# Kernel tuning notes

Measured on AMD Instinct MI355X. Metric: run time of the kernel, lower is better.

The kernel has to match this reference:

```python
import jax, jax.numpy as jnp
import numpy as np

NUM_ITERS = 15
EPSILON = 0.05
MESH_ITERS = 3


def _cost_proj(x, W1, b1, W2, b2):
    # Linear -> ReLU -> Linear
    h = jax.nn.relu(x @ W1 + b1)
    return h @ W2 + b2


def setup_inputs() -> dict:
    key = jax.random.key(0)
    ks = jax.random.split(key, 4)
    B, K, M, D = 8192, 32, 32, 256
    s = 1.0 / np.sqrt(D)
    return {
        "slots_q": jax.random.normal(ks[0], (B, K, D), dtype=jnp.float32),
        "slots_r": jax.random.normal(ks[1], (B, M, D), dtype=jnp.float32),
        "W1": (jax.random.normal(ks[2], (D, D), dtype=jnp.float32) * s),
        "b1": jnp.zeros((D,), dtype=jnp.float32),
        "W2": (jax.random.normal(ks[3], (D, D), dtype=jnp.float32) * s),
        "b2": jnp.zeros((D,), dtype=jnp.float32),
    }


def reference(slots_q, slots_r, W1, b1, W2, b2):
    q = _cost_proj(slots_q, W1, b1, W2, b2)  # [B,K,D]
    r = _cost_proj(slots_r, W1, b1, W2, b2)  # [B,M,D]
    # torch.cdist p=2: pairwise euclidean distance
    sq = (jnp.sum(q * q, -1)[:, :, None]
          + jnp.sum(r * r, -1)[:, None, :]
          - 2.0 * jnp.einsum('bkd,bmd->bkm', q, r))
    C = jnp.sqrt(jnp.clip(sq, 0.0))  # [B,K,M]
    B, K, M = C.shape
    log_K = -C / EPSILON
    log_a = jnp.zeros((B, K, 1), dtype=C.dtype)
    log_b = jnp.zeros((B, 1, M), dtype=C.dtype)
    for _ in range(NUM_ITERS):
        log_a = -jax.nn.logsumexp(log_K + log_b, axis=2, keepdims=True)
        log_b = -jax.nn.logsumexp(log_K + log_a, axis=1, keepdims=True)
    T = jnp.exp(log_K + log_a + log_b)
    for _ in range(MESH_ITERS):
        T = T ** 2
        T = T / (jnp.sum(T, axis=-1, keepdims=True) + 1e-8)
        T = T / (jnp.sum(T, axis=-2, keepdims=True) + 1e-8)
    cost = jnp.sum(T * C, axis=(-1, -2))  # [B]
    similarity = jax.nn.sigmoid(-cost)
    return similarity, T, C, cost
```

## Files before the change

kernel.cpp:

```cpp
#include <hip/hip_runtime.h>


typedef unsigned short u16;
typedef short short8 __attribute__((ext_vector_type(8)));
typedef float f32x4  __attribute__((ext_vector_type(4)));

#define MFMA(a, b, c) __builtin_amdgcn_mfma_f32_16x16x32_bf16((a), (b), (c), 0, 0, 0)

static __device__ __forceinline__ u16 f2bf(float f) {
  unsigned u = __float_as_uint(f);
  return (u16)((u + 0x7FFFu + ((u >> 16) & 1u)) >> 16);
}
static __device__ __forceinline__ float bf2f(u16 h) {
  return __uint_as_float(((unsigned)h) << 16);
}

__global__ __launch_bounds__(256) void prep_w(const float* __restrict__ W1,
                                              const float* __restrict__ W2,
                                              u16* __restrict__ ws) {
  int id = blockIdx.x * 256 + threadIdx.x;
  int mat = id >> 16;
  int e = id & 65535;
  int k = e >> 8, n = e & 255;
  float wv = (mat ? W2 : W1)[e];
  int ki = k >> 5, kl = k & 31;
  int g = kl >> 3, j = kl & 7;
  int lane = g * 16 + (n & 15);
  int ctg = n >> 4;
  ws[mat * 65536 + ((((ki * 16 + ctg) * 64 + lane) << 3) | j)] = f2bf(wv);
}

struct __align__(16) SMemA {
  u16 F[16384];
  float nrm[64];
};

static __device__ __forceinline__ void gemm_frag(const u16* __restrict__ Af,
                                                 const u16* __restrict__ wf,
                                                 int w, int lane, f32x4 acc[4][2]) {
#pragma unroll
  for (int rt = 0; rt < 4; ++rt) {
    acc[rt][0] = f32x4{0.f, 0.f, 0.f, 0.f};
    acc[rt][1] = f32x4{0.f, 0.f, 0.f, 0.f};
  }
#pragma unroll
  for (int ki = 0; ki < 8; ++ki) {
    const u16* bp = wf + (((ki * 16 + 2 * w) * 64 + lane) << 3);
    short8 b0 = *reinterpret_cast<const short8*>(bp);
    short8 b1 = *reinterpret_cast<const short8*>(bp + 512);
    short8 a[4];
#pragma unroll
    for (int rt = 0; rt < 4; ++rt)
      a[rt] = *reinterpret_cast<const short8*>(Af + (((ki * 4 + rt) * 64 + lane) << 3));
#pragma unroll
    for (int rt = 0; rt < 4; ++rt) {
      acc[rt][0] = MFMA(a[rt], b0, acc[rt][0]);
      acc[rt][1] = MFMA(a[rt], b1, acc[rt][1]);
    }
  }
}

__global__ __launch_bounds__(512, 8) void gemm_cdist(
    const float* __restrict__ slots_q, const float* __restrict__ slots_r,
    const float* __restrict__ b1, const float* __restrict__ b2,
    const u16* __restrict__ ws, float* __restrict__ CO) {
  __shared__ SMemA sm;
  const int tid = threadIdx.x, b = blockIdx.x;
  const int w = tid >> 6, lane = tid & 63, g = lane >> 4, ln = lane & 15;

  {
    const float* srcq = slots_q + (size_t)b * 8192;
    const float* srcr = slots_r + (size_t)b * 8192;
#pragma unroll
    for (int ii = 0; ii < 4; ++ii) {
      int s = tid + ii * 512;
      int ki = s >> 8, rt = (s >> 6) & 3, sg = (s >> 4) & 3, sln = s & 15;
      int row = rt * 16 + sln;
      const float* src = (row < 32) ? (srcq + row * 256) : (srcr + (row - 32) * 256);
      int k0 = ki * 32 + sg * 8;
      float4 v0 = *reinterpret_cast<const float4*>(src + k0);
      float4 v1 = *reinterpret_cast<const float4*>(src + k0 + 4);
      short8 o;
      o[0] = (short)f2bf(v0.x); o[1] = (short)f2bf(v0.y);
      o[2] = (short)f2bf(v0.z); o[3] = (short)f2bf(v0.w);
      o[4] = (short)f2bf(v1.x); o[5] = (short)f2bf(v1.y);
      o[6] = (short)f2bf(v1.z); o[7] = (short)f2bf(v1.w);
      *reinterpret_cast<short8*>(&sm.F[s << 3]) = o;
    }
  }
  float bv1a = b1[32 * w + ln], bv1b = b1[32 * w + 16 + ln];
  float bv2a = b2[32 * w + ln], bv2b = b2[32 * w + 16 + ln];
  __syncthreads();

  f32x4 acc[4][2];
  gemm_frag(sm.F, ws, w, lane, acc);
  __syncthreads();
#pragma unroll
  for (int ct = 0; ct < 2; ++ct) {
    float bv = ct ? bv1b : bv1a;
#pragma unroll
    for (int rt = 0; rt < 4; ++rt)
#pragma unroll
      for (int ri = 0; ri < 4; ++ri) {
        int lane2 = (2 * ct + (ln >> 3)) * 16 + 4 * g + ri;
        sm.F[(((w * 4 + rt) * 64 + lane2) << 3) | (ln & 7)] =
            f2bf(fmaxf(acc[rt][ct][ri] + bv, 0.0f));
      }
  }
  __syncthreads();

  gemm_frag(sm.F, ws + 65536, w, lane, acc);
  __syncthreads();
#pragma unroll
  for (int ct = 0; ct < 2; ++ct) {
    float bv = ct ? bv2b : bv2a;
#pragma unroll
    for (int rt = 0; rt < 4; ++rt)
#pragma unroll
      for (int ri = 0; ri < 4; ++ri) {
        int lane2 = (2 * ct + (ln >> 3)) * 16 + 4 * g + ri;
        sm.F[(((w * 4 + rt) * 64 + lane2) << 3) | (ln & 7)] =
            f2bf(acc[rt][ct][ri] + bv);
      }
  }
  __syncthreads();

  f32x4 dacc = f32x4{0.f, 0.f, 0.f, 0.f};
  if (w < 4) {
    const int mt = w >> 1, nt = w & 1;
#pragma unroll
    for (int ki = 0; ki < 8; ++ki) {
      short8 aq = *reinterpret_cast<const short8*>(
          &sm.F[(((ki * 4 + mt) * 64 + lane) << 3)]);
      short8 br = *reinterpret_cast<const short8*>(
          &sm.F[(((ki * 4 + 2 + nt) * 64 + lane) << 3)]);
      dacc = MFMA(aq, br, dacc);
    }
  } else {
    const int t = w - 4;
    float s = 0.f;
#pragma unroll
    for (int ki = 0; ki < 8; ++ki) {
      short8 v = *reinterpret_cast<const short8*>(
          &sm.F[(((ki * 4 + t) * 64 + lane) << 3)]);
#pragma unroll
      for (int i = 0; i < 8; ++i) {
        float f = bf2f((u16)v[i]);
        s = fmaf(f, f, s);
      }
    }
    s += __shfl_xor(s, 16);
    s += __shfl_xor(s, 32);
    if (lane < 16) sm.nrm[t * 16 + lane] = s;
  }
  __syncthreads();

  if (w < 4) {
    const int mt = w >> 1, nt = w & 1;
    float* Cp = CO + (size_t)b * 1024;
#pragma unroll
    for (int ri = 0; ri < 4; ++ri) {
      int k = mt * 16 + 4 * g + ri;
      int m = nt * 16 + ln;
      float sq = sm.nrm[k] + sm.nrm[32 + m] - 2.0f * dacc[ri];
      Cp[k * 32 + m] = sqrtf(fmaxf(sq, 0.0f));
    }
  }
}

__global__ __launch_bounds__(256, 4) void sinkhorn_mesh(
    const float* __restrict__ CO, float* __restrict__ simO,
    float* __restrict__ TO, float* __restrict__ costO, int Bn) {
  __shared__ float Wl[4][32 * 33];
  __shared__ float ABl[4][64];
  const int wv = threadIdx.x >> 6, lane = threadIdx.x & 63;
  const int p = blockIdx.x * 4 + wv;
  if (p >= Bn) return;
  const int h = lane >> 5, q = lane & 31;
  float* Wm = Wl[wv];
  float* LA = ABl[wv];
  float* LB = ABl[wv] + 32;
  const float* Cp = CO + (size_t)p * 1024;

  float lkr[16], lkc[16];
#pragma unroll
  for (int jj = 0; jj < 4; ++jj) {
    float4 v = *reinterpret_cast<const float4*>(Cp + q * 32 + h * 16 + jj * 4);
    int base = q * 33 + h * 16 + jj * 4;
    Wm[base + 0] = v.x; Wm[base + 1] = v.y; Wm[base + 2] = v.z; Wm[base + 3] = v.w;
    lkr[jj * 4 + 0] = -20.f * v.x; lkr[jj * 4 + 1] = -20.f * v.y;
    lkr[jj * 4 + 2] = -20.f * v.z; lkr[jj * 4 + 3] = -20.f * v.w;
  }
  LB[q] = 0.0f;
  __builtin_amdgcn_wave_barrier();
#pragma unroll
  for (int j = 0; j < 16; ++j) lkc[j] = -20.f * Wm[(h * 16 + j) * 33 + q];

  for (int it = 0; it < 15; ++it) {
    float v[16], mx, s;
#pragma unroll
    for (int j = 0; j < 16; ++j) v[j] = lkr[j] + LB[h * 16 + j];
    mx = v[0];
#pragma unroll
    for (int j = 1; j < 16; ++j) mx = fmaxf(mx, v[j]);
    mx = fmaxf(mx, __shfl_xor(mx, 32));
    s = 0.f;
#pragma unroll
    for (int j = 0; j < 16; ++j) s += __expf(v[j] - mx);
    s += __shfl_xor(s, 32);
    LA[q] = -(mx + __logf(s));
    __builtin_amdgcn_wave_barrier();
#pragma unroll
    for (int j = 0; j < 16; ++j) v[j] = lkc[j] + LA[h * 16 + j];
    mx = v[0];
#pragma unroll
    for (int j = 1; j < 16; ++j) mx = fmaxf(mx, v[j]);
    mx = fmaxf(mx, __shfl_xor(mx, 32));
    s = 0.f;
#pragma unroll
    for (int j = 0; j < 16; ++j) s += __expf(v[j] - mx);
    s += __shfl_xor(s, 32);
    LB[q] = -(mx + __logf(s));
    __builtin_amdgcn_wave_barrier();
  }

  float t[16];
  {
    float la = LA[q];
#pragma unroll
    for (int j = 0; j < 16; ++j) t[j] = __expf(lkr[j] + la + LB[h * 16 + j]);
  }

  for (int mi = 0; mi < 3; ++mi) {
    float s = 0.f;
#pragma unroll
    for (int j = 0; j < 16; ++j) { t[j] *= t[j]; s += t[j]; }
    s += __shfl_xor(s, 32);
    float inv = 1.0f / (s + 1e-8f);
#pragma unroll
    for (int j = 0; j < 16; ++j) Wm[q * 33 + h * 16 + j] = t[j] * inv;
    __builtin_amdgcn_wave_barrier();
#pragma unroll
    for (int j = 0; j < 16; ++j) t[j] = Wm[(h * 16 + j) * 33 + q];
    s = 0.f;
#pragma unroll
    for (int j = 0; j < 16; ++j) s += t[j];
    s += __shfl_xor(s, 32);
    inv = 1.0f / (s + 1e-8f);
#pragma unroll
    for (int j = 0; j < 16; ++j) Wm[(h * 16 + j) * 33 + q] = t[j] * inv;
    __builtin_amdgcn_wave_barrier();
#pragma unroll
    for (int j = 0; j < 16; ++j) t[j] = Wm[q * 33 + h * 16 + j];
  }

  float pp = 0.f;
#pragma unroll
  for (int j = 0; j < 16; ++j) pp = fmaf(t[j], -0.05f * lkr[j], pp);
  pp += __shfl_xor(pp, 1); pp += __shfl_xor(pp, 2); pp += __shfl_xor(pp, 4);
  pp += __shfl_xor(pp, 8); pp += __shfl_xor(pp, 16); pp += __shfl_xor(pp, 32);
  if (lane == 0) {
    costO[p] = pp;
    simO[p] = 1.0f / (1.0f + __expf(pp));
  }
#pragma unroll
  for (int jj = 0; jj < 4; ++jj) {
    float4 o;
    o.x = t[jj * 4 + 0]; o.y = t[jj * 4 + 1];
    o.z = t[jj * 4 + 2]; o.w = t[jj * 4 + 3];
    *reinterpret_cast<float4*>(TO + (size_t)p * 1024 + q * 32 + h * 16 + jj * 4) = o;
  }
}

extern "C" void kernel_launch(void* const* d_in, const int* in_sizes, int n_in,
                              void* d_out, int out_size, void* d_ws, size_t ws_size,
                              hipStream_t stream) {
  const float* slots_q = (const float*)d_in[0];
  const float* slots_r = (const float*)d_in[1];
  const float* W1 = (const float*)d_in[2];
  const float* b1 = (const float*)d_in[3];
  const float* W2 = (const float*)d_in[4];
  const float* b2 = (const float*)d_in[5];
  float* out = (float*)d_out;

  const int Bn = in_sizes[0] / 8192;
  u16* ws = (u16*)d_ws;

  prep_w<<<dim3(512), dim3(256), 0, stream>>>(W1, W2, ws);

  float* simO = out;
  float* TO = out + Bn;
  float* CO = TO + (size_t)Bn * 1024;
  float* costO = CO + (size_t)Bn * 1024;

  gemm_cdist<<<dim3(Bn), dim3(512), 0, stream>>>(slots_q, slots_r, b1, b2, ws, CO);
  sinkhorn_mesh<<<dim3((Bn + 3) / 4), dim3(256), 0, stream>>>(CO, simO, TO, costO, Bn);
}
```

Before: 261.6 us.

## Process four batches per block with register-prefetched input and MFMA priority

Result: slower. 815.8 us (+211.8%).

```diff
diff --git a/kernel.cpp b/kernel.cpp
--- a/kernel.cpp
+++ b/kernel.cpp
@@ -43,6 +43,7 @@
     acc[rt][0] = f32x4{0.f, 0.f, 0.f, 0.f};
     acc[rt][1] = f32x4{0.f, 0.f, 0.f, 0.f};
   }
+  __builtin_amdgcn_s_setprio(1);
 #pragma unroll
   for (int ki = 0; ki < 8; ++ki) {
     const u16* bp = wf + (((ki * 16 + 2 * w) * 64 + lane) << 3);
@@ -58,112 +59,138 @@
       acc[rt][1] = MFMA(a[rt], b1, acc[rt][1]);
     }
   }
-}
-
-__global__ __launch_bounds__(512, 8) void gemm_cdist(
+  __builtin_amdgcn_s_setprio(0);
+}
+
+__global__ __launch_bounds__(512, 6) void gemm_cdist(
     const float* __restrict__ slots_q, const float* __restrict__ slots_r,
     const float* __restrict__ b1, const float* __restrict__ b2,
-    const u16* __restrict__ ws, float* __restrict__ CO) {
+    const u16* __restrict__ ws, float* __restrict__ CO, int Bn) {
   __shared__ SMemA sm;
-  const int tid = threadIdx.x, b = blockIdx.x;
+  const int tid = threadIdx.x;
   const int w = tid >> 6, lane = tid & 63, g = lane >> 4, ln = lane & 15;
 
-  {
-    const float* srcq = slots_q + (size_t)b * 8192;
-    const float* srcr = slots_r + (size_t)b * 8192;
+  const int pb0 = blockIdx.x * 4;
+  if (pb0 >= Bn) return;
+  const int npb = (Bn - pb0 < 4) ? (Bn - pb0) : 4;
+
+  const float bv1a = b1[32 * w + ln], bv1b = b1[32 * w + 16 + ln];
+  const float bv2a = b2[32 * w + ln], bv2b = b2[32 * w + 16 + ln];
+
+  const float* sp[4];
+#pragma unroll
+  for (int ii = 0; ii < 4; ++ii) {
+    int s = tid + ii * 512;
+    int ki = s >> 8, rt = (s >> 6) & 3, sg = (s >> 4) & 3, sln = s & 15;
+    int row = rt * 16 + sln;
+    int k0 = ki * 32 + sg * 8;
+    sp[ii] = ((row < 32) ? (slots_q + row * 256) : (slots_r + (row - 32) * 256)) +
+             (size_t)pb0 * 8192 + k0;
+  }
+
+  float4 fl[8];
+#pragma unroll
+  for (int ii = 0; ii < 4; ++ii) {
+    fl[2 * ii]     = *reinterpret_cast<const float4*>(sp[ii]);
+    fl[2 * ii + 1] = *reinterpret_cast<const float4*>(sp[ii] + 4);
+    sp[ii] += 8192;
+  }
+
+  for (int p = 0; p < npb; ++p) {
 #pragma unroll
     for (int ii = 0; ii < 4; ++ii) {
-      int s = tid + ii * 512;
-      int ki = s >> 8, rt = (s >> 6) & 3, sg = (s >> 4) & 3, sln = s & 15;
-      int row = rt * 16 + sln;
-      const float* src = (row < 32) ? (srcq + row * 256) : (srcr + (row - 32) * 256);
-      int k0 = ki * 32 + sg * 8;
-      float4 v0 = *reinterpret_cast<const float4*>(src + k0);
-      float4 v1 = *reinterpret_cast<const float4*>(src + k0 + 4);
       short8 o;
-      o[0] = (short)f2bf(v0.x); o[1] = (short)f2bf(v0.y);
-      o[2] = (short)f2bf(v0.z); o[3] = (short)f2bf(v0.w);
-      o[4] = (short)f2bf(v1.x); o[5] = (short)f2bf(v1.y);
-      o[6] = (short)f2bf(v1.z); o[7] = (short)f2bf(v1.w);
-      *reinterpret_cast<short8*>(&sm.F[s << 3]) = o;
-    }
-  }
-  float bv1a = b1[32 * w + ln], bv1b = b1[32 * w + 16 + ln];
-  float bv2a = b2[32 * w + ln], bv2b = b2[32 * w + 16 + ln];
-  __syncthreads();
-
-  f32x4 acc[4][2];
-  gemm_frag(sm.F, ws, w, lane, acc);
-  __syncthreads();
-#pragma unroll
-  for (int ct = 0; ct < 2; ++ct) {
-    float bv = ct ? bv1b : bv1a;
-#pragma unroll
-    for (int rt = 0; rt < 4; ++rt)
+      o[0] = (short)f2bf(fl[2 * ii].x);     o[1] = (short)f2bf(fl[2 * ii].y);
+      o[2] = (short)f2bf(fl[2 * ii].z);     o[3] = (short)f2bf(fl[2 * ii].w);
+      o[4] = (short)f2bf(fl[2 * ii + 1].x); o[5] = (short)f2bf(fl[2 * ii + 1].y);
+      o[6] = (short)f2bf(fl[2 * ii + 1].z); o[7] = (short)f2bf(fl[2 * ii + 1].w);
+      *reinterpret_cast<short8*>(&sm.F[(tid + ii * 512) << 3]) = o;
+    }
+    __syncthreads();
+
+    f32x4 acc[4][2];
+    gemm_frag(sm.F, ws, w, lane, acc);
+    __syncthreads();
+#pragma unroll
+    for (int ct = 0; ct < 2; ++ct) {
+      float bv = ct ? bv1b : bv1a;
+#pragma unroll
+      for (int rt = 0; rt < 4; ++rt)
+#pragma unroll
+        for (int ri = 0; ri < 4; ++ri) {
+          int lane2 = (2 * ct + (ln >> 3)) * 16 + 4 * g + ri;
+          sm.F[(((w * 4 + rt) * 64 + lane2) << 3) | (ln & 7)] =
+              f2bf(fmaxf(acc[rt][ct][ri] + bv, 0.0f));
+        }
+    }
+    __syncthreads();
+
+    gemm_frag(sm.F, ws + 65536, w, lane, acc);
+    __syncthreads();
+#pragma unroll
+    for (int ct = 0; ct < 2; ++ct) {
+      float bv = ct ? bv2b : bv2a;
+#pragma unroll
+      for (int rt = 0; rt < 4; ++rt)
+#pragma unroll
+        for (int ri = 0; ri < 4; ++ri) {
+          int lane2 = (2 * ct + (ln >> 3)) * 16 + 4 * g + ri;
+          sm.F[(((w * 4 + rt) * 64 + lane2) << 3) | (ln & 7)] =
+              f2bf(acc[rt][ct][ri] + bv);
+        }
+    }
+    if (p + 1 < npb) {
+#pragma unroll
+      for (int ii = 0; ii < 4; ++ii) {
+        fl[2 * ii]     = *reinterpret_cast<const float4*>(sp[ii]);
+        fl[2 * ii + 1] = *reinterpret_cast<const float4*>(sp[ii] + 4);
+        sp[ii] += 8192;
+      }
+    }
+    __syncthreads();
+
+    f32x4 dacc = f32x4{0.f, 0.f, 0.f, 0.f};
+    if (w < 4) {
+      const int mt = w >> 1, nt = w & 1;
+      __builtin_amdgcn_s_setprio(1);
+#pragma unroll
+      for (int ki = 0; ki < 8; ++ki) {
+        short8 aq = *reinterpret_cast<const short8*>(
+            &sm.F[(((ki * 4 + mt) * 64 + lane) << 3)]);
+        short8 br = *reinterpret_cast<const short8*>(
+            &sm.F[(((ki * 4 + 2 + nt) * 64 + lane) << 3)]);
+        dacc = MFMA(aq, br, dacc);
+      }
+      __builtin_amdgcn_s_setprio(0);
+    } else {
+      const int t = w - 4;
+      float s = 0.f;
+#pragma unroll
+      for (int ki = 0; ki < 8; ++ki) {
+        short8 v = *reinterpret_cast<const short8*>(
+            &sm.F[(((ki * 4 + t) * 64 + lane) << 3)]);
+#pragma unroll
+        for (int i = 0; i < 8; ++i) {
+          float f = bf2f((u16)v[i]);
+          s = fmaf(f, f, s);
+        }
+      }
+      s += __shfl_xor(s, 16);
+      s += __shfl_xor(s, 32);
+      if (lane < 16) sm.nrm[t * 16 + lane] = s;
+    }
+    __syncthreads();
+
+    if (w < 4) {
+      const int mt = w >> 1, nt = w & 1;
+      float* Cp = CO + (size_t)(pb0 + p) * 1024;
 #pragma unroll
       for (int ri = 0; ri < 4; ++ri) {
-        int lane2 = (2 * ct + (ln >> 3)) * 16 + 4 * g + ri;
-        sm.F[(((w * 4 + rt) * 64 + lane2) << 3) | (ln & 7)] =
-            f2bf(fmaxf(acc[rt][ct][ri] + bv, 0.0f));
+        int k = mt * 16 + 4 * g + ri;
+        int m = nt * 16 + ln;
+        float sq = sm.nrm[k] + sm.nrm[32 + m] - 2.0f * dacc[ri];
+        Cp[k * 32 + m] = sqrtf(fmaxf(sq, 0.0f));
       }
-  }
-  __syncthreads();
-
-  gemm_frag(sm.F, ws + 65536, w, lane, acc);
-  __syncthreads();
-#pragma unroll
-  for (int ct = 0; ct < 2; ++ct) {
-    float bv = ct ? bv2b : bv2a;
-#pragma unroll
-    for (int rt = 0; rt < 4; ++rt)
-#pragma unroll
-      for (int ri = 0; ri < 4; ++ri) {
-        int lane2 = (2 * ct + (ln >> 3)) * 16 + 4 * g + ri;
-        sm.F[(((w * 4 + rt) * 64 + lane2) << 3) | (ln & 7)] =
-            f2bf(acc[rt][ct][ri] + bv);
-      }
-  }
-  __syncthreads();
-
-  f32x4 dacc = f32x4{0.f, 0.f, 0.f, 0.f};
-  if (w < 4) {
-    const int mt = w >> 1, nt = w & 1;
-#pragma unroll
-    for (int ki = 0; ki < 8; ++ki) {
-      short8 aq = *reinterpret_cast<const short8*>(
-          &sm.F[(((ki * 4 + mt) * 64 + lane) << 3)]);
-      short8 br = *reinterpret_cast<const short8*>(
-          &sm.F[(((ki * 4 + 2 + nt) * 64 + lane) << 3)]);
-      dacc = MFMA(aq, br, dacc);
-    }
-  } else {
-    const int t = w - 4;
-    float s = 0.f;
-#pragma unroll
-    for (int ki = 0; ki < 8; ++ki) {
-      short8 v = *reinterpret_cast<const short8*>(
-          &sm.F[(((ki * 4 + t) * 64 + lane) << 3)]);
-#pragma unroll
-      for (int i = 0; i < 8; ++i) {
-        float f = bf2f((u16)v[i]);
-        s = fmaf(f, f, s);
-      }
-    }
-    s += __shfl_xor(s, 16);
-    s += __shfl_xor(s, 32);
-    if (lane < 16) sm.nrm[t * 16 + lane] = s;
-  }
-  __syncthreads();
-
-  if (w < 4) {
-    const int mt = w >> 1, nt = w & 1;
-    float* Cp = CO + (size_t)b * 1024;
-#pragma unroll
-    for (int ri = 0; ri < 4; ++ri) {
-      int k = mt * 16 + 4 * g + ri;
-      int m = nt * 16 + ln;
-      float sq = sm.nrm[k] + sm.nrm[32 + m] - 2.0f * dacc[ri];
-      Cp[k * 32 + m] = sqrtf(fmaxf(sq, 0.0f));
     }
   }
 }
@@ -293,6 +320,7 @@
   float* CO = TO + (size_t)Bn * 1024;
   float* costO = CO + (size_t)Bn * 1024;
 
-  gemm_cdist<<<dim3(Bn), dim3(512), 0, stream>>>(slots_q, slots_r, b1, b2, ws, CO);
+  gemm_cdist<<<dim3((Bn + 3) / 4), dim3(512), 0, stream>>>(slots_q, slots_r,
+                                                           b1, b2, ws, CO, Bn);
   sinkhorn_mesh<<<dim3((Bn + 3) / 4), dim3(256), 0, stream>>>(CO, simO, TO, costO, Bn);
 }
```
